# Optimization experiments

Measured on AMD Instinct MI355X. Metric: run time of the kernel, lower is better.

Reference implementation:

```python
import jax, jax.numpy as jnp
import numpy as np


def setup_inputs() -> dict:
    key = jax.random.key(0)
    B, D = 1024, 65536
    inputs = jax.random.normal(key, (B, D), dtype=jnp.float32)
    return {"inputs": inputs, "k": 1024}


def reference(inputs, k):
    # top_k along last axis (matches tf.math.top_k)
    top_k_vals, _ = jax.lax.top_k(inputs, k)          # [B, k]
    # tf.math.reduce_min with no axis -> global scalar threshold
    threshold = jnp.min(top_k_vals)
    mask = jnp.where(inputs >= threshold, jnp.float32(1.0), jnp.float32(0.0))
    return mask * inputs
```

## Files before the change

### kernel.cpp

```cpp
#include <hip/hip_runtime.h>
#include <stdint.h>

#define TPB 256
#define NBH 2048
#define NB3 1024
#define CAP 6144
#define DCOLS 65536
#define NSAMP 4096

typedef float f4 __attribute__((ext_vector_type(4)));

__device__ __forceinline__ unsigned f2key(float f) {
  unsigned u = __float_as_uint(f);
  unsigned m = ((int)u >> 31) | 0x80000000u;
  return u ^ m;
}
__device__ __forceinline__ float key2f(unsigned k) {
  unsigned u = (k & 0x80000000u) ? (k ^ 0x80000000u) : ~k;
  return __uint_as_float(u);
}

__device__ __forceinline__ void clear_hist(unsigned* hist, int NB) {
  for (int i = threadIdx.x; i < NB; i += TPB) hist[i] = 0u;
}

__device__ void find_top(const unsigned* hist, int NB, unsigned K,
                         unsigned* scan, unsigned* selbin, unsigned* selrem) {
  const int tid = threadIdx.x;
  const int C = NB / TPB;
  unsigned cs = 0;
  for (int i = 0; i < C; ++i) cs += hist[tid * C + i];
  scan[tid] = cs;
  __syncthreads();
  if (tid < 64) {
    unsigned e0 = scan[tid * 4 + 0], e1 = scan[tid * 4 + 1];
    unsigned e2 = scan[tid * 4 + 2], e3 = scan[tid * 4 + 3];
    unsigned s = e0 + e1 + e2 + e3;
    unsigned suff = s;
    for (int off = 1; off < 64; off <<= 1) {
      unsigned t = __shfl_down(suff, off);
      if (tid + off < 64) suff += t;
    }
    unsigned tail = suff - s;
    scan[tid * 4 + 3] = e3 + tail;
    scan[tid * 4 + 2] = e2 + e3 + tail;
    scan[tid * 4 + 1] = e1 + e2 + e3 + tail;
    scan[tid * 4 + 0] = s + tail;
  }
  __syncthreads();
  unsigned suff = scan[tid];
  unsigned above = suff - cs;
  if (above < K && suff >= K) {
    unsigned cAbove = above;
    for (int bin = tid * C + C - 1; bin >= tid * C; --bin) {
      unsigned c = hist[bin];
      if (cAbove + c >= K) { *selbin = (unsigned)bin; *selrem = K - cAbove; break; }
      cAbove += c;
    }
  }
  __syncthreads();
}

__global__ void __launch_bounds__(TPB)
topk_select(const float* __restrict__ in, const int* __restrict__ kptr,
            unsigned* __restrict__ rowkey) {
  __shared__ unsigned hist[NBH];
  __shared__ unsigned scan[TPB];
  __shared__ unsigned cand[CAP];
  __shared__ unsigned sel_bin, sel_rem, cand_cnt;

  const int tid = threadIdx.x;
  const int lane = tid & 63;
  const int row = blockIdx.x;
  const unsigned K = (unsigned)(*kptr);
  const f4* rowv = (const f4*)(in + (size_t)row * DCOLS);
  const int n4 = DCOLS / 4;

  clear_hist(hist, NBH);
  if (tid == 0) cand_cnt = 0u;
  __syncthreads();
  for (int j = 0; j < NSAMP / 4 / TPB; ++j) {
    f4 v = rowv[tid + j * TPB];
    atomicAdd(&hist[f2key(v.x) >> 21], 1u);
    atomicAdd(&hist[f2key(v.y) >> 21], 1u);
    atomicAdd(&hist[f2key(v.z) >> 21], 1u);
    atomicAdd(&hist[f2key(v.w) >> 21], 1u);
  }
  __syncthreads();
  unsigned ksamp = K >> 3;
  if (ksamp < 32u) ksamp = 32u;
  if (ksamp > NSAMP - 1) ksamp = NSAMP - 1;
  find_top(hist, NBH, ksamp, scan, &sel_bin, &sel_rem);
  const unsigned tlo = sel_bin << 21;
  __syncthreads();

  for (int i = tid; i < n4; i += TPB) {
    f4 v = rowv[i];
    unsigned kx = f2key(v.x), ky = f2key(v.y), kz = f2key(v.z), kw = f2key(v.w);
#define CPCT(kk)                                                               \
    {                                                                          \
      bool p = (kk) >= tlo;                                                    \
      unsigned long long m = __ballot(p);                                      \
      if (m) {                                                                 \
        unsigned base = 0;                                                     \
        if (lane == 0) base = atomicAdd(&cand_cnt, (unsigned)__popcll(m));     \
        base = __shfl(base, 0);                                                \
        if (p) {                                                               \
          unsigned off = base + (unsigned)__popcll(m & ((1ull << lane) - 1ull));\
          if (off < CAP) cand[off] = (kk);                                     \
        }                                                                      \
      }                                                                        \
    }
    CPCT(kx) CPCT(ky) CPCT(kz) CPCT(kw)
#undef CPCT
  }
  __syncthreads();
  const unsigned nc = cand_cnt;
  __syncthreads();

  if (nc >= K && nc <= CAP) {
    clear_hist(hist, NBH); __syncthreads();
    for (unsigned i = tid; i < nc; i += TPB) atomicAdd(&hist[cand[i] >> 21], 1u);
    __syncthreads();
    find_top(hist, NBH, K, scan, &sel_bin, &sel_rem);
    const unsigned b1 = sel_bin, K2 = sel_rem;
    __syncthreads();

    clear_hist(hist, NBH); __syncthreads();
    for (unsigned i = tid; i < nc; i += TPB) {
      unsigned kk = cand[i];
      if ((kk >> 21) == b1) atomicAdd(&hist[(kk >> 10) & (NBH - 1)], 1u);
    }
    __syncthreads();
    find_top(hist, NBH, K2, scan, &sel_bin, &sel_rem);
    const unsigned b2 = sel_bin, K3 = sel_rem;
    __syncthreads();

    clear_hist(hist, NB3); __syncthreads();
    const unsigned pfx = (b1 << 11) | b2;
    for (unsigned i = tid; i < nc; i += TPB) {
      unsigned kk = cand[i];
      if ((kk >> 10) == pfx) atomicAdd(&hist[kk & (NB3 - 1)], 1u);
    }
    __syncthreads();
    find_top(hist, NB3, K3, scan, &sel_bin, &sel_rem);
    if (tid == 0) rowkey[row] = (b1 << 21) | (b2 << 10) | sel_bin;
  } else {
    clear_hist(hist, NBH); __syncthreads();
    for (int i = tid; i < n4; i += TPB) {
      f4 v = rowv[i];
      atomicAdd(&hist[f2key(v.x) >> 21], 1u);
      atomicAdd(&hist[f2key(v.y) >> 21], 1u);
      atomicAdd(&hist[f2key(v.z) >> 21], 1u);
      atomicAdd(&hist[f2key(v.w) >> 21], 1u);
    }
    __syncthreads();
    find_top(hist, NBH, K, scan, &sel_bin, &sel_rem);
    const unsigned b1 = sel_bin, K2 = sel_rem;
    __syncthreads();

    clear_hist(hist, NBH); __syncthreads();
    for (int i = tid; i < n4; i += TPB) {
      f4 v = rowv[i];
      unsigned kk;
      kk = f2key(v.x); if ((kk >> 21) == b1) atomicAdd(&hist[(kk >> 10) & (NBH - 1)], 1u);
      kk = f2key(v.y); if ((kk >> 21) == b1) atomicAdd(&hist[(kk >> 10) & (NBH - 1)], 1u);
      kk = f2key(v.z); if ((kk >> 21) == b1) atomicAdd(&hist[(kk >> 10) & (NBH - 1)], 1u);
      kk = f2key(v.w); if ((kk >> 21) == b1) atomicAdd(&hist[(kk >> 10) & (NBH - 1)], 1u);
    }
    __syncthreads();
    find_top(hist, NBH, K2, scan, &sel_bin, &sel_rem);
    const unsigned b2 = sel_bin, K3 = sel_rem;
    __syncthreads();

    clear_hist(hist, NB3); __syncthreads();
    const unsigned pfx = (b1 << 11) | b2;
    for (int i = tid; i < n4; i += TPB) {
      f4 v = rowv[i];
      unsigned kk;
      kk = f2key(v.x); if ((kk >> 10) == pfx) atomicAdd(&hist[kk & (NB3 - 1)], 1u);
      kk = f2key(v.y); if ((kk >> 10) == pfx) atomicAdd(&hist[kk & (NB3 - 1)], 1u);
      kk = f2key(v.z); if ((kk >> 10) == pfx) atomicAdd(&hist[kk & (NB3 - 1)], 1u);
      kk = f2key(v.w); if ((kk >> 10) == pfx) atomicAdd(&hist[kk & (NB3 - 1)], 1u);
    }
    __syncthreads();
    find_top(hist, NB3, K3, scan, &sel_bin, &sel_rem);
    if (tid == 0) rowkey[row] = (b1 << 21) | (b2 << 10) | sel_bin;
  }
}

__global__ void __launch_bounds__(TPB)
minreduce(const unsigned* __restrict__ rowkey, unsigned* __restrict__ thr, int n) {
  __shared__ unsigned s[TPB];
  unsigned m = 0xFFFFFFFFu;
  for (int i = threadIdx.x; i < n; i += TPB) m = min(m, rowkey[i]);
  s[threadIdx.x] = m;
  __syncthreads();
  for (int off = TPB / 2; off > 0; off >>= 1) {
    if (threadIdx.x < off) s[threadIdx.x] = min(s[threadIdx.x], s[threadIdx.x + off]);
    __syncthreads();
  }
  if (threadIdx.x == 0) thr[0] = s[0];
}

__global__ void __launch_bounds__(TPB)
maskk(const f4* __restrict__ in, f4* __restrict__ out,
      const unsigned* __restrict__ thrkey, int n4) {
  const float thr = key2f(thrkey[0]);
  int idx = blockIdx.x * TPB + threadIdx.x;
  int stride = gridDim.x * TPB;
  for (int i = idx; i < n4; i += stride) {
    f4 v = in[i];
    f4 o;
    o.x = (v.x >= thr) ? v.x : 0.0f;
    o.y = (v.y >= thr) ? v.y : 0.0f;
    o.z = (v.z >= thr) ? v.z : 0.0f;
    o.w = (v.w >= thr) ? v.w : 0.0f;
    __builtin_nontemporal_store(o, &out[i]);
  }
}

extern "C" void kernel_launch(void* const* d_in, const int* in_sizes, int n_in,
                              void* d_out, int out_size, void* d_ws, size_t ws_size,
                              hipStream_t stream) {
  const float* in = (const float*)d_in[0];
  const int* kptr = (const int*)d_in[1];
  f4* out = (f4*)d_out;
  unsigned* rowkey = (unsigned*)d_ws;
  unsigned* thr = rowkey + 1024;

  const int B = in_sizes[0] / DCOLS;
  const int n4 = out_size / 4;

  hipLaunchKernelGGL(topk_select, dim3(B), dim3(TPB), 0, stream, in, kptr, rowkey);
  hipLaunchKernelGGL(minreduce, dim3(1), dim3(TPB), 0, stream, rowkey, thr, B);
  hipLaunchKernelGGL(maskk, dim3(4096), dim3(TPB), 0, stream,
                     (const f4*)in, out, thr, n4);
}
```

Measured before the change: 486.5 us.

## Unroll candidate scan with wave-level early skip and fuse min-reduce via atomicMin

The compaction pass now issues four independent float4 loads per iteration, giving more memory-level parallelism. A wave-wide ballot skips all four ballot/atomic compaction steps when no lane has a value above the sample threshold. The separate minreduce kernel is replaced by an atomicMin on a global threshold that a memset initialises, which removes one kernel launch. Launch bounds now request 4 waves per EU, which may limit registers for the unrolled loads.

```diff
diff --git a/kernel.cpp b/kernel.cpp
--- a/kernel.cpp
+++ b/kernel.cpp
@@ -61,9 +61,9 @@
   __syncthreads();
 }
 
-__global__ void __launch_bounds__(TPB)
+__global__ void __launch_bounds__(TPB, 4)
 topk_select(const float* __restrict__ in, const int* __restrict__ kptr,
-            unsigned* __restrict__ rowkey) {
+            unsigned* __restrict__ thr) {
   __shared__ unsigned hist[NBH];
   __shared__ unsigned scan[TPB];
   __shared__ unsigned cand[CAP];
@@ -79,12 +79,16 @@
   clear_hist(hist, NBH);
   if (tid == 0) cand_cnt = 0u;
   __syncthreads();
-  for (int j = 0; j < NSAMP / 4 / TPB; ++j) {
-    f4 v = rowv[tid + j * TPB];
-    atomicAdd(&hist[f2key(v.x) >> 21], 1u);
-    atomicAdd(&hist[f2key(v.y) >> 21], 1u);
-    atomicAdd(&hist[f2key(v.z) >> 21], 1u);
+  {
+    f4 s0 = rowv[tid], s1 = rowv[tid + TPB];
+    f4 s2 = rowv[tid + 2 * TPB], s3 = rowv[tid + 3 * TPB];
+#define HSAMP(v)                                                               \
+    atomicAdd(&hist[f2key(v.x) >> 21], 1u);                                    \
+    atomicAdd(&hist[f2key(v.y) >> 21], 1u);                                    \
+    atomicAdd(&hist[f2key(v.z) >> 21], 1u);                                    \
     atomicAdd(&hist[f2key(v.w) >> 21], 1u);
+    HSAMP(s0) HSAMP(s1) HSAMP(s2) HSAMP(s3)
+#undef HSAMP
   }
   __syncthreads();
   unsigned ksamp = K >> 3;
@@ -94,9 +98,6 @@
   const unsigned tlo = sel_bin << 21;
   __syncthreads();
 
-  for (int i = tid; i < n4; i += TPB) {
-    f4 v = rowv[i];
-    unsigned kx = f2key(v.x), ky = f2key(v.y), kz = f2key(v.z), kw = f2key(v.w);
 #define CPCT(kk)                                                               \
     {                                                                          \
       bool p = (kk) >= tlo;                                                    \
@@ -111,13 +112,26 @@
         }                                                                      \
       }                                                                        \
     }
-    CPCT(kx) CPCT(ky) CPCT(kz) CPCT(kw)
-#undef CPCT
-  }
+#define PROC(v)                                                                \
+    {                                                                          \
+      unsigned kx = f2key(v.x), ky = f2key(v.y);                               \
+      unsigned kz = f2key(v.z), kw = f2key(v.w);                               \
+      bool any = (kx >= tlo) | (ky >= tlo) | (kz >= tlo) | (kw >= tlo);        \
+      if (__ballot(any)) { CPCT(kx) CPCT(ky) CPCT(kz) CPCT(kw) }               \
+    }
+  for (int base = 0; base < n4; base += TPB * 4) {
+    f4 v0 = rowv[base + tid];
+    f4 v1 = rowv[base + tid + TPB];
+    f4 v2 = rowv[base + tid + 2 * TPB];
+    f4 v3 = rowv[base + tid + 3 * TPB];
+    PROC(v0) PROC(v1) PROC(v2) PROC(v3)
+  }
+#undef PROC
   __syncthreads();
   const unsigned nc = cand_cnt;
   __syncthreads();
 
+  unsigned rk;
   if (nc >= K && nc <= CAP) {
     clear_hist(hist, NBH); __syncthreads();
     for (unsigned i = tid; i < nc; i += TPB) atomicAdd(&hist[cand[i] >> 21], 1u);
@@ -144,7 +158,7 @@
     }
     __syncthreads();
     find_top(hist, NB3, K3, scan, &sel_bin, &sel_rem);
-    if (tid == 0) rowkey[row] = (b1 << 21) | (b2 << 10) | sel_bin;
+    rk = (b1 << 21) | (b2 << 10) | sel_bin;
   } else {
     clear_hist(hist, NBH); __syncthreads();
     for (int i = tid; i < n4; i += TPB) {
@@ -185,22 +199,10 @@
     }
     __syncthreads();
     find_top(hist, NB3, K3, scan, &sel_bin, &sel_rem);
-    if (tid == 0) rowkey[row] = (b1 << 21) | (b2 << 10) | sel_bin;
-  }
-}
-
-__global__ void __launch_bounds__(TPB)
-minreduce(const unsigned* __restrict__ rowkey, unsigned* __restrict__ thr, int n) {
-  __shared__ unsigned s[TPB];
-  unsigned m = 0xFFFFFFFFu;
-  for (int i = threadIdx.x; i < n; i += TPB) m = min(m, rowkey[i]);
-  s[threadIdx.x] = m;
-  __syncthreads();
-  for (int off = TPB / 2; off > 0; off >>= 1) {
-    if (threadIdx.x < off) s[threadIdx.x] = min(s[threadIdx.x], s[threadIdx.x + off]);
-    __syncthreads();
-  }
-  if (threadIdx.x == 0) thr[0] = s[0];
+    rk = (b1 << 21) | (b2 << 10) | sel_bin;
+  }
+#undef CPCT
+  if (tid == 0) atomicMin(thr, rk);
 }
 
 __global__ void __launch_bounds__(TPB)
@@ -226,14 +228,13 @@
   const float* in = (const float*)d_in[0];
   const int* kptr = (const int*)d_in[1];
   f4* out = (f4*)d_out;
-  unsigned* rowkey = (unsigned*)d_ws;
-  unsigned* thr = rowkey + 1024;
+  unsigned* thr = (unsigned*)d_ws;
 
   const int B = in_sizes[0] / DCOLS;
   const int n4 = out_size / 4;
 
-  hipLaunchKernelGGL(topk_select, dim3(B), dim3(TPB), 0, stream, in, kptr, rowkey);
-  hipLaunchKernelGGL(minreduce, dim3(1), dim3(TPB), 0, stream, rowkey, thr, B);
+  hipMemsetAsync(thr, 0xFF, 4, stream);
+  hipLaunchKernelGGL(topk_select, dim3(B), dim3(TPB), 0, stream, in, kptr, thr);
   hipLaunchKernelGGL(maskk, dim3(4096), dim3(TPB), 0, stream,
                      (const f4*)in, out, thr, n4);
 }
```

Result: no change. 482.9 us (-0.7%).
